# Performance work log

Measured on AMD Instinct MI355X. Metric: run time of the kernel, lower is better.

## Reference

```python
import jax, jax.numpy as jnp
import numpy as np

D_IN, D_OUT = 768, 64
SCALE = 1.0 / np.sqrt(D_OUT)

def setup_inputs() -> dict:
    key = jax.random.key(0)
    kx, kq, kk, kv = jax.random.split(key, 4)
    B, S = 4, 4096
    x = jax.random.normal(kx, (B, S, D_IN), dtype=jnp.float32)
    # torch Linear weights are [out, in]; we store transposed [in, out] for x @ W
    init = 1.0 / np.sqrt(D_IN)
    Wq = jax.random.uniform(kq, (D_IN, D_OUT), jnp.float32, -init, init)
    Wk = jax.random.uniform(kk, (D_IN, D_OUT), jnp.float32, -init, init)
    Wv = jax.random.uniform(kv, (D_IN, D_OUT), jnp.float32, -init, init)
    return {"x": x, "Wq": Wq, "Wk": Wk, "Wv": Wv}

def reference(x, Wq, Wk, Wv):
    # x: [B, S, D_IN]
    q = x @ Wq  # [B, S, D_OUT]
    k = x @ Wk
    v = x @ Wv
    scores = jnp.einsum('bqd,bkd->bqk', q, k)  # [B, S, S]
    S = x.shape[1]
    causal = jnp.triu(jnp.ones((S, S), dtype=bool), k=1)
    scores = jnp.where(causal, -jnp.inf, scores)
    attn = jax.nn.softmax(scores * SCALE, axis=-1)
    # dropout_percentage=0.0 -> identity
    return jnp.einsum('bqk,bkd->bqd', attn, v)
```

## Files before the change

kernel.cpp:

```cpp
#include <hip/hip_runtime.h>

typedef unsigned short u16;
typedef unsigned int u32;
typedef __attribute__((ext_vector_type(4))) float f32x4;
typedef __attribute__((ext_vector_type(8))) short s16x8;
typedef __attribute__((ext_vector_type(4))) u16 u16x4;
typedef __attribute__((ext_vector_type(4))) u32 u32x4;

#define SCALE_LOG2E (0.125f * 1.44269504088896340736f)
#define NEGBIG (-3.0e38f)

__device__ inline u16 f2bf(float f) {
  u32 u = __builtin_bit_cast(u32, f);
  u += 0x7fffu + ((u >> 16) & 1u);
  return (u16)(u >> 16);
}

__global__ void wconv_kernel(const float* __restrict__ Wq, const float* __restrict__ Wk,
                             const float* __restrict__ Wv, u16* __restrict__ Wt) {
  int base = blockIdx.x * 1024 + threadIdx.x;
  #pragma unroll
  for (int i = 0; i < 4; ++i) {
    int idx = base + i * 256;
    int n = idx / 768, k = idx - n * 768;
    int m = n >> 6, c = n & 63;
    const float* W = (m == 0) ? Wq : (m == 1 ? Wk : Wv);
    float v = W[k * 64 + c];
    if (m == 0) v *= SCALE_LOG2E;
    Wt[idx] = f2bf(v);
  }
}

__global__ __launch_bounds__(512) void proj_kernel(const float* __restrict__ x,
                                                   const u16* __restrict__ Wt,
                                                   u16* __restrict__ Qs,
                                                   u16* __restrict__ Kb,
                                                   u16* __restrict__ Vt) {
  __shared__ __align__(16) u16 xT[64 * 64];
  __shared__ __align__(16) u16 Wl[192 * 64];

  const int t = threadIdx.x;
  const int lane = t & 63;
  const int wv = t >> 6;
  const int c15 = lane & 15, g = lane >> 4;
  const int mg = wv >> 1, nh = wv & 1;
  const int m0 = blockIdx.x * 64;

  f32x4 acc[6];
  #pragma unroll
  for (int f = 0; f < 6; ++f) acc[f] = 0.0f;

  const int xr = t >> 3;
  const int xc = (t & 7) * 8;

  for (int kt = 0; kt < 12; ++kt) {
    const int k0 = kt * 64;
    const float* xp = x + (size_t)(m0 + xr) * 768 + k0 + xc;
    f32x4 a0 = *(const f32x4*)(xp);
    f32x4 a1 = *(const f32x4*)(xp + 4);
    u32x4 wch[3];
    #pragma unroll
    for (int i = 0; i < 3; ++i) {
      int ci = t + i * 512;
      int rw = ci >> 3, ch = ci & 7;
      wch[i] = *(const u32x4*)(Wt + rw * 768 + k0 + ch * 8);
    }
    __syncthreads();
    {
      u32x4 px;
      px.x = (u32)f2bf(a0.x) | ((u32)f2bf(a0.y) << 16);
      px.y = (u32)f2bf(a0.z) | ((u32)f2bf(a0.w) << 16);
      px.z = (u32)f2bf(a1.x) | ((u32)f2bf(a1.y) << 16);
      px.w = (u32)f2bf(a1.z) | ((u32)f2bf(a1.w) << 16);
      int ch = t & 7;
      int sw = ch ^ (xr & 7);
      *(u32x4*)(&xT[xr * 64 + sw * 8]) = px;
    }
    #pragma unroll
    for (int i = 0; i < 3; ++i) {
      int ci = t + i * 512;
      int rw = ci >> 3, ch = ci & 7;
      int sw = ch ^ (rw & 7);
      *(u32x4*)(&Wl[rw * 64 + sw * 8]) = wch[i];
    }
    __syncthreads();
    #pragma unroll
    for (int kk = 0; kk < 2; ++kk) {
      const int arow = 16 * mg + c15;
      s16x8 af = *(const s16x8*)(&xT[arow * 64 + (((kk * 4 + g) ^ (arow & 7)) * 8)]);
      #pragma unroll
      for (int f = 0; f < 6; ++f) {
        const int brow = 96 * nh + 16 * f + c15;
        s16x8 bf = *(const s16x8*)(&Wl[brow * 64 + (((kk * 4 + g) ^ (brow & 7)) * 8)]);
        acc[f] = __builtin_amdgcn_mfma_f32_16x16x32_bf16(af, bf, acc[f], 0, 0, 0);
      }
    }
  }

  const int b = m0 >> 12;
  const int s0 = m0 & 4095;
  const int mbase = m0 + 16 * mg + 4 * g;
  #pragma unroll
  for (int f = 0; f < 6; ++f) {
    const int n16 = 96 * nh + 16 * f;
    if (n16 < 64) {
      const int coln = n16 + c15;
      #pragma unroll
      for (int j = 0; j < 4; ++j)
        Qs[(size_t)(mbase + j) * 64 + coln] = f2bf(acc[f][j]);
    } else if (n16 < 128) {
      const int coln = n16 - 64 + c15;
      #pragma unroll
      for (int j = 0; j < 4; ++j)
        Kb[(size_t)(mbase + j) * 64 + coln] = f2bf(acc[f][j]);
    } else {
      const int d = n16 - 128 + c15;
      u16x4 pk;
      pk.x = f2bf(acc[f][0]); pk.y = f2bf(acc[f][1]);
      pk.z = f2bf(acc[f][2]); pk.w = f2bf(acc[f][3]);
      *(u16x4*)(Vt + (size_t)(b * 64 + d) * 4096 + s0 + 16 * mg + 4 * g) = pk;
    }
  }
}

__global__ __launch_bounds__(256) void attn_kernel(const u16* __restrict__ Qs,
                                                   const u16* __restrict__ Kb,
                                                   const u16* __restrict__ Vt,
                                                   float* __restrict__ out) {
  __shared__ __align__(16) char smem[4 * 32 * 64 * 4 + 2 * 4 * 32 * 4];
  float* osl = (float*)smem;
  float* msh = (float*)(smem + 32768);
  float* lsh = (float*)(smem + 32768 + 512);

  const int t = threadIdx.x;
  const int lane = t & 63;
  const int w = t >> 6;
  const int c15 = lane & 15, g = lane >> 4;
  const int bid = blockIdx.x;
  const int qb = 127 - (bid >> 2);
  const int b = bid & 3;
  const int q0 = qb * 32;

  u16* P = (u16*)smem + w * (32 * 72);

  const u16* Qb  = Qs + (size_t)b * 4096 * 64;
  const u16* Kbb = Kb + (size_t)b * 4096 * 64;
  const u16* Vtb = Vt + (size_t)b * 64 * 4096;

  s16x8 qf[2][2];
  #pragma unroll
  for (int r = 0; r < 2; ++r)
    #pragma unroll
    for (int kk = 0; kk < 2; ++kk)
      qf[r][kk] = *(const s16x8*)(Qb + (size_t)(q0 + 16 * r + c15) * 64 + 32 * kk + 8 * g);

  f32x4 o[2][4];
  float mrow[2][4], lrow[2][4];
  #pragma unroll
  for (int r = 0; r < 2; ++r)
    #pragma unroll
    for (int j = 0; j < 4; ++j) {
      o[r][j] = 0.0f; mrow[r][j] = NEGBIG; lrow[r][j] = 0.0f;
    }

  const int T = (qb >> 1) + 1;
  for (int tile = w; tile < T; tile += 4) {
    const int kv0 = tile * 64;
    f32x4 s[2][4];
    #pragma unroll
    for (int r = 0; r < 2; ++r)
      #pragma unroll
      for (int f = 0; f < 4; ++f) s[r][f] = 0.0f;
    #pragma unroll
    for (int kk = 0; kk < 2; ++kk) {
      s16x8 kf[4];
      #pragma unroll
      for (int f = 0; f < 4; ++f)
        kf[f] = *(const s16x8*)(Kbb + (size_t)(kv0 + 16 * f + c15) * 64 + 32 * kk + 8 * g);
      #pragma unroll
      for (int r = 0; r < 2; ++r)
        #pragma unroll
        for (int f = 0; f < 4; ++f)
          s[r][f] = __builtin_amdgcn_mfma_f32_16x16x32_bf16(qf[r][kk], kf[f], s[r][f], 0, 0, 0);
    }
    if (kv0 + 63 > q0) {
      #pragma unroll
      for (int r = 0; r < 2; ++r)
        #pragma unroll
        for (int f = 0; f < 4; ++f) {
          const int kcol = kv0 + 16 * f + c15;
          #pragma unroll
          for (int j = 0; j < 4; ++j) {
            const int qrow = q0 + 16 * r + 4 * g + j;
            if (kcol > qrow) s[r][f][j] = NEGBIG;
          }
        }
    }
    #pragma unroll
    for (int r = 0; r < 2; ++r)
      #pragma unroll
      for (int j = 0; j < 4; ++j) {
        float mx = fmaxf(fmaxf(s[r][0][j], s[r][1][j]), fmaxf(s[r][2][j], s[r][3][j]));
        mx = fmaxf(mx, __shfl_xor(mx, 1));
        mx = fmaxf(mx, __shfl_xor(mx, 2));
        mx = fmaxf(mx, __shfl_xor(mx, 4));
        mx = fmaxf(mx, __shfl_xor(mx, 8));
        const float mn = fmaxf(mrow[r][j], mx);
        const float al = exp2f(mrow[r][j] - mn);
        float ps[4], sum = 0.0f;
        #pragma unroll
        for (int f = 0; f < 4; ++f) { ps[f] = exp2f(s[r][f][j] - mn); sum += ps[f]; }
        sum += __shfl_xor(sum, 1);
        sum += __shfl_xor(sum, 2);
        sum += __shfl_xor(sum, 4);
        sum += __shfl_xor(sum, 8);
        lrow[r][j] = lrow[r][j] * al + sum;
        mrow[r][j] = mn;
        #pragma unroll
        for (int fd = 0; fd < 4; ++fd) o[r][fd][j] *= al;
        const int prow = 16 * r + 4 * g + j;
        #pragma unroll
        for (int f = 0; f < 4; ++f) {
          const float pn = __shfl_xor(ps[f], 1);
          if (!(lane & 1)) {
            const u32 pk = (u32)f2bf(ps[f]) | ((u32)f2bf(pn) << 16);
            *(u32*)(&P[prow * 72 + 16 * f + c15]) = pk;
          }
        }
      }
    #pragma unroll
    for (int kk = 0; kk < 2; ++kk) {
      s16x8 pa[2];
      #pragma unroll
      for (int r = 0; r < 2; ++r)
        pa[r] = *(const s16x8*)(&P[(16 * r + c15) * 72 + 32 * kk + 8 * g]);
      s16x8 vf[4];
      #pragma unroll
      for (int f = 0; f < 4; ++f)
        vf[f] = *(const s16x8*)(Vtb + (size_t)(16 * f + c15) * 4096 + kv0 + 32 * kk + 8 * g);
      #pragma unroll
      for (int r = 0; r < 2; ++r)
        #pragma unroll
        for (int f = 0; f < 4; ++f)
          o[r][f] = __builtin_amdgcn_mfma_f32_16x16x32_bf16(pa[r], vf[f], o[r][f], 0, 0, 0);
    }
  }

  __syncthreads();

  if (c15 == 0) {
    #pragma unroll
    for (int r = 0; r < 2; ++r)
      #pragma unroll
      for (int j = 0; j < 4; ++j) {
        const int row = 16 * r + 4 * g + j;
        msh[w * 32 + row] = mrow[r][j];
        lsh[w * 32 + row] = lrow[r][j];
      }
  }
  #pragma unroll
  for (int r = 0; r < 2; ++r)
    #pragma unroll
    for (int f = 0; f < 4; ++f)
      #pragma unroll
      for (int j = 0; j < 4; ++j) {
        const int row = 16 * r + 4 * g + j;
        osl[(w * 32 + row) * 64 + 16 * f + c15] = o[r][f][j];
      }
  __syncthreads();

  {
    const int row = t >> 3;
    const int cb = (t & 7) * 8;
    float m0v = msh[row], m1v = msh[32 + row], m2v = msh[64 + row], m3v = msh[96 + row];
    float M = fmaxf(fmaxf(m0v, m1v), fmaxf(m2v, m3v));
    float a0 = exp2f(m0v - M), a1 = exp2f(m1v - M), a2 = exp2f(m2v - M), a3 = exp2f(m3v - M);
    float L = a0 * lsh[row] + a1 * lsh[32 + row] + a2 * lsh[64 + row] + a3 * lsh[96 + row];
    const float inv = 1.0f / L;
    float* op = out + (size_t)(b * 4096 + q0 + row) * 64 + cb;
    #pragma unroll
    for (int c = 0; c < 8; ++c) {
      float v = a0 * osl[(row) * 64 + cb + c] + a1 * osl[(32 + row) * 64 + cb + c] +
                a2 * osl[(64 + row) * 64 + cb + c] + a3 * osl[(96 + row) * 64 + cb + c];
      op[c] = v * inv;
    }
  }
}

extern "C" void kernel_launch(void* const* d_in, const int* in_sizes, int n_in,
                              void* d_out, int out_size, void* d_ws, size_t ws_size,
                              hipStream_t stream) {
  const float* x  = (const float*)d_in[0];
  const float* Wq = (const float*)d_in[1];
  const float* Wk = (const float*)d_in[2];
  const float* Wv = (const float*)d_in[3];
  float* out = (float*)d_out;

  char* ws = (char*)d_ws;
  u16* Wt = (u16*)(ws);
  u16* Qs = (u16*)(ws + 524288);
  u16* Kb = (u16*)(ws + 2621440);
  u16* Vt = (u16*)(ws + 4718592);

  wconv_kernel<<<144, 256, 0, stream>>>(Wq, Wk, Wv, Wt);
  proj_kernel<<<256, 512, 0, stream>>>(x, Wt, Qs, Kb, Vt);
  attn_kernel<<<512, 256, 0, stream>>>(Qs, Kb, Vt, out);
}
```

Baseline: 193.4 us.

## Prefetch next K-tile in projection and use 8 waves per attention block

The projection kernel now loads the next 64-wide chunk of x and the weights into registers while the current chunk sits in shared memory, overlapping global loads with MFMA work. The attention kernel doubles its block to 512 threads (8 waves), each wave striding over KV tiles by 8. Partial softmax states are merged in two steps: waves 4-7 spill to shared memory and waves 0-3 fold them in before the final 4-way reduction. This spreads the causal KV loop over more waves to cut per-block latency, at the cost of an extra reduction pass, more synchronisation and register pressure from launch_bounds(512,4).

```diff
diff --git a/kernel.cpp b/kernel.cpp
--- a/kernel.cpp
+++ b/kernel.cpp
@@ -53,18 +53,21 @@
   const int xr = t >> 3;
   const int xc = (t & 7) * 8;
 
-  for (int kt = 0; kt < 12; ++kt) {
-    const int k0 = kt * 64;
-    const float* xp = x + (size_t)(m0 + xr) * 768 + k0 + xc;
-    f32x4 a0 = *(const f32x4*)(xp);
-    f32x4 a1 = *(const f32x4*)(xp + 4);
-    u32x4 wch[3];
+  f32x4 a0, a1;
+  u32x4 wch[3];
+  {
+    const float* xp = x + (size_t)(m0 + xr) * 768 + xc;
+    a0 = *(const f32x4*)(xp);
+    a1 = *(const f32x4*)(xp + 4);
     #pragma unroll
     for (int i = 0; i < 3; ++i) {
       int ci = t + i * 512;
       int rw = ci >> 3, ch = ci & 7;
-      wch[i] = *(const u32x4*)(Wt + rw * 768 + k0 + ch * 8);
-    }
+      wch[i] = *(const u32x4*)(Wt + rw * 768 + ch * 8);
+    }
+  }
+
+  for (int kt = 0; kt < 12; ++kt) {
     __syncthreads();
     {
       u32x4 px;
@@ -83,6 +86,18 @@
       int sw = ch ^ (rw & 7);
       *(u32x4*)(&Wl[rw * 64 + sw * 8]) = wch[i];
     }
+    if (kt < 11) {
+      const int k0 = (kt + 1) * 64;
+      const float* xp = x + (size_t)(m0 + xr) * 768 + k0 + xc;
+      a0 = *(const f32x4*)(xp);
+      a1 = *(const f32x4*)(xp + 4);
+      #pragma unroll
+      for (int i = 0; i < 3; ++i) {
+        int ci = t + i * 512;
+        int rw = ci >> 3, ch = ci & 7;
+        wch[i] = *(const u32x4*)(Wt + rw * 768 + k0 + ch * 8);
+      }
+    }
     __syncthreads();
     #pragma unroll
     for (int kk = 0; kk < 2; ++kk) {
@@ -123,11 +138,11 @@
   }
 }
 
-__global__ __launch_bounds__(256) void attn_kernel(const u16* __restrict__ Qs,
-                                                   const u16* __restrict__ Kb,
-                                                   const u16* __restrict__ Vt,
-                                                   float* __restrict__ out) {
-  __shared__ __align__(16) char smem[4 * 32 * 64 * 4 + 2 * 4 * 32 * 4];
+__global__ __launch_bounds__(512, 4) void attn_kernel(const u16* __restrict__ Qs,
+                                                      const u16* __restrict__ Kb,
+                                                      const u16* __restrict__ Vt,
+                                                      float* __restrict__ out) {
+  __shared__ __align__(16) char smem[8 * 32 * 72 * 2];
   float* osl = (float*)smem;
   float* msh = (float*)(smem + 32768);
   float* lsh = (float*)(smem + 32768 + 512);
@@ -164,7 +179,7 @@
     }
 
   const int T = (qb >> 1) + 1;
-  for (int tile = w; tile < T; tile += 4) {
+  for (int tile = w; tile < T; tile += 8) {
     const int kv0 = tile * 64;
     f32x4 s[2][4];
     #pragma unroll
@@ -248,30 +263,72 @@
 
   __syncthreads();
 
-  if (c15 == 0) {
+  if (w >= 4) {
+    const int ws = w - 4;
+    if (c15 == 0) {
+      #pragma unroll
+      for (int r = 0; r < 2; ++r)
+        #pragma unroll
+        for (int j = 0; j < 4; ++j) {
+          const int row = 16 * r + 4 * g + j;
+          msh[ws * 32 + row] = mrow[r][j];
+          lsh[ws * 32 + row] = lrow[r][j];
+        }
+    }
+    #pragma unroll
+    for (int r = 0; r < 2; ++r)
+      #pragma unroll
+      for (int f = 0; f < 4; ++f)
+        #pragma unroll
+        for (int j = 0; j < 4; ++j) {
+          const int row = 16 * r + 4 * g + j;
+          osl[(ws * 32 + row) * 64 + 16 * f + c15] = o[r][f][j];
+        }
+  }
+  __syncthreads();
+
+  if (w < 4) {
     #pragma unroll
     for (int r = 0; r < 2; ++r)
       #pragma unroll
       for (int j = 0; j < 4; ++j) {
         const int row = 16 * r + 4 * g + j;
-        msh[w * 32 + row] = mrow[r][j];
-        lsh[w * 32 + row] = lrow[r][j];
+        const float mp = msh[w * 32 + row];
+        const float lp = lsh[w * 32 + row];
+        const float mn = fmaxf(mrow[r][j], mp);
+        const float aa = exp2f(mrow[r][j] - mn);
+        const float ab = exp2f(mp - mn);
+        #pragma unroll
+        for (int f = 0; f < 4; ++f)
+          o[r][f][j] = o[r][f][j] * aa + osl[(w * 32 + row) * 64 + 16 * f + c15] * ab;
+        lrow[r][j] = lrow[r][j] * aa + lp * ab;
+        mrow[r][j] = mn;
       }
-  }
-  #pragma unroll
-  for (int r = 0; r < 2; ++r)
-    #pragma unroll
-    for (int f = 0; f < 4; ++f)
-      #pragma unroll
-      for (int j = 0; j < 4; ++j) {
-        const int row = 16 * r + 4 * g + j;
-        osl[(w * 32 + row) * 64 + 16 * f + c15] = o[r][f][j];
-      }
+    if (c15 == 0) {
+      #pragma unroll
+      for (int r = 0; r < 2; ++r)
+        #pragma unroll
+        for (int j = 0; j < 4; ++j) {
+          const int row = 16 * r + 4 * g + j;
+          msh[w * 32 + row] = mrow[r][j];
+          lsh[w * 32 + row] = lrow[r][j];
+        }
+    }
+    #pragma unroll
+    for (int r = 0; r < 2; ++r)
+      #pragma unroll
+      for (int f = 0; f < 4; ++f)
+        #pragma unroll
+        for (int j = 0; j < 4; ++j) {
+          const int row = 16 * r + 4 * g + j;
+          osl[(w * 32 + row) * 64 + 16 * f + c15] = o[r][f][j];
+        }
+  }
   __syncthreads();
 
   {
-    const int row = t >> 3;
-    const int cb = (t & 7) * 8;
+    const int row = t >> 4;
+    const int cb = (t & 15) * 4;
     float m0v = msh[row], m1v = msh[32 + row], m2v = msh[64 + row], m3v = msh[96 + row];
     float M = fmaxf(fmaxf(m0v, m1v), fmaxf(m2v, m3v));
     float a0 = exp2f(m0v - M), a1 = exp2f(m1v - M), a2 = exp2f(m2v - M), a3 = exp2f(m3v - M);
@@ -279,7 +336,7 @@
     const float inv = 1.0f / L;
     float* op = out + (size_t)(b * 4096 + q0 + row) * 64 + cb;
     #pragma unroll
-    for (int c = 0; c < 8; ++c) {
+    for (int c = 0; c < 4; ++c) {
       float v = a0 * osl[(row) * 64 + cb + c] + a1 * osl[(32 + row) * 64 + cb + c] +
                 a2 * osl[(64 + row) * 64 + cb + c] + a3 * osl[(96 + row) * 64 + cb + c];
       op[c] = v * inv;
@@ -304,5 +361,5 @@
 
   wconv_kernel<<<144, 256, 0, stream>>>(Wq, Wk, Wv, Wt);
   proj_kernel<<<256, 512, 0, stream>>>(x, Wt, Qs, Kb, Vt);
-  attn_kernel<<<512, 256, 0, stream>>>(Qs, Kb, Vt, out);
-}
+  attn_kernel<<<512, 512, 0, stream>>>(Qs, Kb, Vt, out);
+}
```

New measurement: 184.7 us. -4.5%, faster.
